# Optimization experiments

Measured on AMD Instinct MI355X. Metric: run time of the kernel, lower is better.

Reference implementation:

```python
import jax, jax.numpy as jnp
import numpy as np

MISSING_VALUE = 128.0
B, T, D, H = 512, 256, 128, 512

def setup_inputs() -> dict:
    key = jax.random.key(0)
    ks = jax.random.split(key, 12)
    x = jax.random.normal(ks[0], (B, T, D), dtype=jnp.float32)
    miss = jax.random.uniform(ks[1], (B, T, D)) < 0.2
    x = jnp.where(miss, jnp.float32(MISSING_VALUE), x)
    tn = lambda k, shp: (jax.random.truncated_normal(k, -2.0, 2.0, shp, jnp.float32) * 0.1)
    # Keras LSTMCell params: kernel [in, 4H], recurrent_kernel [H, 4H], bias [4H] (gate order i,f,c,o)
    k0 = tn(ks[2], (D, 4 * H)); r0 = tn(ks[3], (H, 4 * H)); b0 = jnp.zeros((4 * H,), jnp.float32)
    k1 = tn(ks[4], (H, 4 * H)); r1 = tn(ks[5], (H, 4 * H)); b1 = jnp.zeros((4 * H,), jnp.float32)
    W = tn(ks[6], (H, D))
    b_out = jnp.full((D,), 0.1, jnp.float32)
    return {"x": x, "k0": k0, "r0": r0, "b0": b0, "k1": k1, "r1": r1, "b1": b1, "W": W, "b_out": b_out}

def _lstm_cell(kern, rec, bias, x_in, h, c):
    z = x_in @ kern + h @ rec + bias  # [B, 4H]
    i, f, g, o = jnp.split(z, 4, axis=-1)
    i = jax.nn.sigmoid(i); f = jax.nn.sigmoid(f); g = jnp.tanh(g); o = jax.nn.sigmoid(o)
    c = f * c + i * g
    h = o * jnp.tanh(c)
    return h, c

def reference(x, k0, r0, b0, k1, r1, b1, W, b_out):
    Bx, Tx, Dx = x.shape
    Hx = r0.shape[0]
    zeros = jnp.zeros((Bx, Hx), x.dtype)
    def step(carry, inp):
        t, x_t = inp
        h0, c0, h1, c1, prev_top = carry
        pred = prev_top @ W + b_out                      # imputation from previous top-layer output
        mask = (x_t == MISSING_VALUE) & (t > 0)          # no imputation at t == 0
        cur = jnp.where(mask, pred, x_t)
        h0, c0 = _lstm_cell(k0, r0, b0, cur, h0, c0)
        h1, c1 = _lstm_cell(k1, r1, b1, h0, h1, c1)
        return (h0, c0, h1, c1, h1), h1
    init = (zeros, zeros, zeros, zeros, zeros)
    _, outs = jax.lax.scan(step, init, (jnp.arange(Tx), jnp.transpose(x, (1, 0, 2))))  # outs: [T, B, H]
    last_cell = outs[-1]
    # tf.concat(outputs[:-1], axis=1) -> [B, (T-1)*H]; reshape -> [B*(T-1), H]
    hid = jnp.transpose(outs[:-1], (1, 0, 2)).reshape(-1, Hx)
    prediction = hid @ W + b_out
    return prediction, last_cell
```

## Files before the change

kernel.cpp:

```cpp
#include <hip/hip_runtime.h>

#define B_ 512
#define T_ 256
#define D_ 128
#define H_ 512

typedef _Float16 f16x8 __attribute__((ext_vector_type(8)));
typedef float f32x4 __attribute__((ext_vector_type(4)));
typedef unsigned long long u64;

__device__ __forceinline__ float sigm(float x) { return 1.f / (1.f + __expf(-x)); }
__device__ __forceinline__ float tanh_(float x) { return 2.f / (1.f + __expf(-2.f * x)) - 1.f; }

__global__ void k_convert(const float* __restrict__ k0, const float* __restrict__ r0,
                          const float* __restrict__ k1, const float* __restrict__ r1,
                          const float* __restrict__ W,
                          _Float16* __restrict__ wB0T,
                          _Float16* __restrict__ wB1T,
                          _Float16* __restrict__ wWT)
{
    int tid = blockIdx.x * blockDim.x + threadIdx.x;
    int nth = gridDim.x * blockDim.x;
    for (int idx = tid; idx < 640 * 2048; idx += nth) {
        int k = idx >> 11, n = idx & 2047;
        float v = (k < 128) ? k0[k * 2048 + n] : r0[(k - 128) * 2048 + n];
        wB0T[n * 640 + k] = (_Float16)v;
    }
    for (int idx = tid; idx < 1024 * 2048; idx += nth) {
        int k = idx >> 11, n = idx & 2047;
        float v = (k < 512) ? k1[k * 2048 + n] : r1[(k - 512) * 2048 + n];
        wB1T[n * 1024 + k] = (_Float16)v;
    }
    for (int idx = tid; idx < 512 * 128; idx += nth) {
        int k = idx >> 7, n = idx & 127;
        wWT[n * 512 + k] = (_Float16)W[k * 128 + n];
    }
}

__global__ void k_init(const float* __restrict__ x, _Float16* __restrict__ cur,
                       _Float16* __restrict__ h0a, _Float16* __restrict__ h0b,
                       _Float16* __restrict__ h1a, _Float16* __restrict__ h1b,
                       float* __restrict__ c0, float* __restrict__ c1)
{
    int tid = blockIdx.x * blockDim.x + threadIdx.x;
    int nth = gridDim.x * blockDim.x;
    for (int idx = tid; idx < B_ * D_; idx += nth) {
        int b = idx >> 7, d = idx & 127;
        cur[idx] = (_Float16)x[b * (T_ * D_) + d];
    }
    for (int idx = tid; idx < B_ * H_; idx += nth) {
        h0a[idx] = (_Float16)0.f; h0b[idx] = (_Float16)0.f;
        h1a[idx] = (_Float16)0.f; h1b[idx] = (_Float16)0.f;
        c0[idx] = 0.f; c1[idx] = 0.f;
    }
}

template <int KTOT, int K1>
__global__ __launch_bounds__(512) void k_layer(
    const _Float16* __restrict__ A1, int lda1,
    const _Float16* __restrict__ A2, int lda2,
    const _Float16* __restrict__ BT,
    const float* __restrict__ bias,
    float* __restrict__ cst,
    _Float16* __restrict__ hout,
    float* __restrict__ hout_f32)
{
    constexpr int LSTR = 144;
    __shared__ __align__(16) char smem[2 * 64 * LSTR * 2];
    _Float16* sA = (_Float16*)smem;
    _Float16* sB = sA + 64 * LSTR;
    float* szred = (float*)smem;

    const int j0 = blockIdx.x * 16;
    const int m0 = blockIdx.y * 64;
    const int tid = threadIdx.x;
    const int lane = tid & 63;
    const int wave = tid >> 6;
    const int wpair = wave >> 1;
    const int ksub = wave & 1;

    const int srow = tid >> 3;
    const int skc = (tid & 7) << 4;
    const int swz = (srow & 7) << 3;
    const int sw1 = srow * LSTR + (skc ^ swz);
    const int sw2 = srow * LSTR + ((skc + 8) ^ swz);
    const int bgrow = (srow >> 4) * 512 + j0 + (srow & 15);

    uint4 rA0, rA1, rB0, rB1;
    auto loadA = [&](int kb) {
        int k = kb + skc;
        const _Float16* a; size_t off;
        if (k < K1) { a = A1; off = (size_t)(m0 + srow) * lda1 + k; }
        else        { a = A2; off = (size_t)(m0 + srow) * lda2 + (k - K1); }
        rA0 = *reinterpret_cast<const uint4*>(a + off);
        rA1 = *reinterpret_cast<const uint4*>(a + off + 8);
    };
    auto loadB = [&](int kb) {
        size_t off = (size_t)bgrow * KTOT + kb + skc;
        rB0 = *reinterpret_cast<const uint4*>(BT + off);
        rB1 = *reinterpret_cast<const uint4*>(BT + off + 8);
    };

    loadA(0); loadB(0);

    f32x4 acc[4] = {};
    const int arow = wpair * 16 + (lane & 15);
    const int abase = arow * LSTR;
    const int aswz = (arow & 7) << 3;
    const int kfrag = ksub * 64 + ((lane >> 4) << 3);

    for (int kb = 0; kb < KTOT; kb += 128) {
        __syncthreads();
        *reinterpret_cast<uint4*>(&sA[sw1]) = rA0;
        *reinterpret_cast<uint4*>(&sA[sw2]) = rA1;
        *reinterpret_cast<uint4*>(&sB[sw1]) = rB0;
        *reinterpret_cast<uint4*>(&sB[sw2]) = rB1;
        if (kb + 128 < KTOT) { loadA(kb + 128); loadB(kb + 128); }
        __syncthreads();
#pragma unroll
        for (int kk = 0; kk < 2; ++kk) {
            int ko = kfrag + kk * 32;
            f16x8 a = *reinterpret_cast<const f16x8*>(&sA[abase + (ko ^ aswz)]);
#pragma unroll
            for (int g = 0; g < 4; ++g) {
                int br = g * 16 + (lane & 15);
                f16x8 b = *reinterpret_cast<const f16x8*>(&sB[br * LSTR + (ko ^ ((br & 7) << 3))]);
                acc[g] = __builtin_amdgcn_mfma_f32_16x16x32_f16(b, a, acc[g], 0, 0, 0);
            }
        }
    }

    __syncthreads();
    if (ksub == 1) {
        float* zr = &szred[(wpair * 64 + lane) * 21];
#pragma unroll
        for (int g = 0; g < 4; ++g)
#pragma unroll
            for (int r = 0; r < 4; ++r)
                zr[g * 4 + r] = acc[g][r];
    }
    __syncthreads();
    if (ksub == 0) {
        const int row  = m0 + wpair * 16 + (lane & 15);
        const int colb = j0 + ((lane >> 4) << 2);
        const float* zr = &szred[(wpair * 64 + lane) * 21];
        f32x4 bi4 = *reinterpret_cast<const f32x4*>(&bias[colb]);
        f32x4 bf4 = *reinterpret_cast<const f32x4*>(&bias[512 + colb]);
        f32x4 bg4 = *reinterpret_cast<const f32x4*>(&bias[1024 + colb]);
        f32x4 bo4 = *reinterpret_cast<const f32x4*>(&bias[1536 + colb]);
        f32x4 c4 = *reinterpret_cast<f32x4*>(&cst[row * H_ + colb]);
        union { _Float16 h[4]; u64 u; } hh;
        f32x4 h4;
#pragma unroll
        for (int r = 0; r < 4; ++r) {
            float zi = acc[0][r] + zr[0 + r] + bi4[r];
            float zf = acc[1][r] + zr[4 + r] + bf4[r];
            float zg = acc[2][r] + zr[8 + r] + bg4[r];
            float zo = acc[3][r] + zr[12 + r] + bo4[r];
            float gi = sigm(zi), gf = sigm(zf), gg = tanh_(zg), go = sigm(zo);
            float c = gf * c4[r] + gi * gg;
            c4[r] = c;
            float h = go * tanh_(c);
            h4[r] = h;
            hh.h[r] = (_Float16)h;
        }
        *reinterpret_cast<f32x4*>(&cst[row * H_ + colb]) = c4;
        *reinterpret_cast<u64*>(&hout[row * H_ + colb]) = hh.u;
        if (hout_f32) *reinterpret_cast<f32x4*>(&hout_f32[row * H_ + colb]) = h4;
    }
}

__global__ __launch_bounds__(512) void k_pred(
    const _Float16* __restrict__ h1prev,
    const _Float16* __restrict__ WT,
    const float* __restrict__ bout,
    const float* __restrict__ x,
    int t,
    _Float16* __restrict__ cur,
    float* __restrict__ outPred)
{
    __shared__ float sred[512 * 5];

    const int tid = threadIdx.x;
    const int wave = tid >> 6, l = tid & 63;
    const int pr = blockIdx.x >> 3;
    const int pc = blockIdx.x & 7;
    const int arow = (pr * 16 + (l & 15)) * 512;
    const int brow = (pc * 16 + (l & 15)) * 512;
    const int kof = (l >> 4) << 3;

    f32x4 acc = {};
#pragma unroll
    for (int kk = 0; kk < 2; ++kk) {
        int k = wave * 64 + kk * 32 + kof;
        f16x8 a = *reinterpret_cast<const f16x8*>(h1prev + arow + k);
        f16x8 b = *reinterpret_cast<const f16x8*>(WT + brow + k);
        acc = __builtin_amdgcn_mfma_f32_16x16x32_f16(b, a, acc, 0, 0, 0);
    }
    {
        float* sr = &sred[(wave * 64 + l) * 5];
#pragma unroll
        for (int r = 0; r < 4; ++r) sr[r] = acc[r];
    }
    __syncthreads();
    if (wave == 0) {
#pragma unroll
        for (int w = 1; w < 8; ++w) {
            const float* sr = &sred[(w * 64 + l) * 5];
#pragma unroll
            for (int r = 0; r < 4; ++r) acc[r] += sr[r];
        }
        const int b = pr * 16 + (l & 15);
        const int colb = pc * 16 + ((l >> 4) << 2);
        f32x4 bo4 = *reinterpret_cast<const f32x4*>(&bout[colb]);
        f32x4 xv4 = *reinterpret_cast<const f32x4*>(&x[((size_t)b * T_ + t) * D_ + colb]);
        f32x4 p4;
        union { _Float16 h[4]; u64 u; } ch;
#pragma unroll
        for (int r = 0; r < 4; ++r) {
            float pred = acc[r] + bo4[r];
            p4[r] = pred;
            float cv = (xv4[r] == 128.0f) ? pred : xv4[r];
            ch.h[r] = (_Float16)cv;
        }
        *reinterpret_cast<f32x4*>(&outPred[((size_t)b * (T_ - 1) + (t - 1)) * D_ + colb]) = p4;
        *reinterpret_cast<u64*>(&cur[b * D_ + colb]) = ch.u;
    }
}

extern "C" void kernel_launch(void* const* d_in, const int* in_sizes, int n_in,
                              void* d_out, int out_size, void* d_ws, size_t ws_size,
                              hipStream_t stream)
{
    const float* x  = (const float*)d_in[0];
    const float* k0 = (const float*)d_in[1];
    const float* r0 = (const float*)d_in[2];
    const float* b0 = (const float*)d_in[3];
    const float* k1 = (const float*)d_in[4];
    const float* r1 = (const float*)d_in[5];
    const float* b1 = (const float*)d_in[6];
    const float* W  = (const float*)d_in[7];
    const float* bo = (const float*)d_in[8];
    float* out = (float*)d_out;

    char* ws = (char*)d_ws;
    size_t off = 0;
    auto alloc = [&](size_t bytes) { void* p = ws + off; off += (bytes + 255) & ~255ull; return p; };
    _Float16* wB0T = (_Float16*)alloc((size_t)2048 * 640 * 2);
    _Float16* wB1T = (_Float16*)alloc((size_t)2048 * 1024 * 2);
    _Float16* wWT  = (_Float16*)alloc((size_t)128 * 512 * 2);
    _Float16* cur  = (_Float16*)alloc((size_t)B_ * D_ * 2);
    _Float16* h0[2] = { (_Float16*)alloc((size_t)B_ * H_ * 2), (_Float16*)alloc((size_t)B_ * H_ * 2) };
    _Float16* h1[2] = { (_Float16*)alloc((size_t)B_ * H_ * 2), (_Float16*)alloc((size_t)B_ * H_ * 2) };
    float* c0 = (float*)alloc((size_t)B_ * H_ * 4);
    float* c1 = (float*)alloc((size_t)B_ * H_ * 4);

    k_convert<<<2048, 256, 0, stream>>>(k0, r0, k1, r1, W, wB0T, wB1T, wWT);
    k_init<<<1024, 256, 0, stream>>>(x, cur, h0[0], h0[1], h1[0], h1[1], c0, c1);

    float* lastcell = out + (size_t)B_ * (T_ - 1) * D_;

    for (int t = 0; t < T_; ++t) {
        int cu = t & 1, pv = cu ^ 1;
        if (t > 0)
            k_pred<<<256, 512, 0, stream>>>(h1[pv], wWT, bo, x, t, cur, out);
        k_layer<640, 128><<<dim3(32, 8), 512, 0, stream>>>(
            cur, D_, h0[pv], H_, wB0T, b0, c0, h0[cu], nullptr);
        k_layer<1024, 512><<<dim3(32, 8), 512, 0, stream>>>(
            h0[cu], H_, h1[pv], H_, wB1T, b1, c1, h1[cu],
            (t == T_ - 1) ? lastcell : nullptr);
    }
}
```

Baseline: 5.134 ms.

## Fuse imputation prediction into layer-0 LSTM kernel with redundant per-block compute

Removes the separate prediction kernel and the global cur buffer. Each layer-0 block recomputes the imputation GEMM for its 64 batch rows and writes the imputed input directly into shared memory, and only column-block 0 writes the prediction output. This drops one kernel launch and a global round trip per timestep. In exchange, the small output GEMM is repeated 32 times across blocks and adds a serial prologue before the main loop.

Result: slower. 8.931 ms (+74.0%).

```diff
diff --git a/kernel.cpp b/kernel.cpp
--- a/kernel.cpp
+++ b/kernel.cpp
@@ -37,21 +37,184 @@
     }
 }
 
-__global__ void k_init(const float* __restrict__ x, _Float16* __restrict__ cur,
-                       _Float16* __restrict__ h0a, _Float16* __restrict__ h0b,
+__global__ void k_init(_Float16* __restrict__ h0a, _Float16* __restrict__ h0b,
                        _Float16* __restrict__ h1a, _Float16* __restrict__ h1b,
                        float* __restrict__ c0, float* __restrict__ c1)
 {
     int tid = blockIdx.x * blockDim.x + threadIdx.x;
     int nth = gridDim.x * blockDim.x;
-    for (int idx = tid; idx < B_ * D_; idx += nth) {
-        int b = idx >> 7, d = idx & 127;
-        cur[idx] = (_Float16)x[b * (T_ * D_) + d];
-    }
     for (int idx = tid; idx < B_ * H_; idx += nth) {
         h0a[idx] = (_Float16)0.f; h0b[idx] = (_Float16)0.f;
         h1a[idx] = (_Float16)0.f; h1b[idx] = (_Float16)0.f;
         c0[idx] = 0.f; c1[idx] = 0.f;
+    }
+}
+
+__global__ __launch_bounds__(512) void k_l0(
+    const _Float16* __restrict__ h1prev,
+    const _Float16* __restrict__ h0prev,
+    const _Float16* __restrict__ WT,
+    const _Float16* __restrict__ B0T,
+    const float* __restrict__ bo,
+    const float* __restrict__ bias,
+    const float* __restrict__ x,
+    int t,
+    float* __restrict__ cst,
+    _Float16* __restrict__ hout,
+    float* __restrict__ outPred)
+{
+    constexpr int LSTR = 144;
+    __shared__ __align__(16) char smem[3 * 64 * LSTR * 2];
+    _Float16* sA = (_Float16*)smem;
+    _Float16* sB = sA + 64 * LSTR;
+    _Float16* cuL = sB + 64 * LSTR;
+    float* szred = (float*)smem;
+
+    const int jx = blockIdx.x;
+    const int j0 = jx * 16;
+    const int m0 = blockIdx.y * 64;
+    const int tid = threadIdx.x;
+    const int lane = tid & 63;
+    const int wave = tid >> 6;
+
+    const int srow = tid >> 3;
+    const int skc = (tid & 7) << 4;
+    const int swz = (srow & 7) << 3;
+    const int sw1 = srow * LSTR + (skc ^ swz);
+    const int sw2 = srow * LSTR + ((skc + 8) ^ swz);
+    const int bgrow = (srow >> 4) * 512 + j0 + (srow & 15);
+
+    uint4 rA0, rA1, rB0, rB1;
+    auto loadB = [&](int kb) {
+        size_t off = (size_t)bgrow * 640 + kb + skc;
+        rB0 = *reinterpret_cast<const uint4*>(B0T + off);
+        rB1 = *reinterpret_cast<const uint4*>(B0T + off + 8);
+    };
+    auto loadA = [&](int kb) {
+        size_t off = (size_t)(m0 + srow) * H_ + (kb - 128) + skc;
+        rA0 = *reinterpret_cast<const uint4*>(h0prev + off);
+        rA1 = *reinterpret_cast<const uint4*>(h0prev + off + 8);
+    };
+    loadB(0);
+
+    if (t == 0) {
+        const int rW = tid >> 3;
+        const int kc0 = (tid & 7) * 16;
+        const int cswz = (rW & 7) << 3;
+#pragma unroll
+        for (int h = 0; h < 2; ++h) {
+            int kc = kc0 + h * 8;
+            union { _Float16 f[8]; uint4 q; } v;
+#pragma unroll
+            for (int e = 0; e < 8; ++e)
+                v.f[e] = (_Float16)x[(size_t)(m0 + rW) * T_ * D_ + kc + e];
+            *reinterpret_cast<uint4*>(&cuL[rW * LSTR + (kc ^ cswz)]) = v.q;
+        }
+    } else {
+        const int msub = wave >> 1;
+        const int cbase = (wave & 1) * 4;
+        const int rW = msub * 16 + (lane & 15);
+        const int gb = m0 + rW;
+        const int kof = (lane >> 4) << 3;
+        f32x4 pacc[4] = {};
+        for (int kb = 0; kb < 512; kb += 32) {
+            int k = kb + kof;
+            f16x8 a = *reinterpret_cast<const f16x8*>(h1prev + (size_t)gb * H_ + k);
+#pragma unroll
+            for (int i = 0; i < 4; ++i) {
+                f16x8 b = *reinterpret_cast<const f16x8*>(
+                    WT + (size_t)((cbase + i) * 16 + (lane & 15)) * 512 + k);
+                pacc[i] = __builtin_amdgcn_mfma_f32_16x16x32_f16(b, a, pacc[i], 0, 0, 0);
+            }
+        }
+        const int cswz = (rW & 7) << 3;
+#pragma unroll
+        for (int i = 0; i < 4; ++i) {
+            int colb = (cbase + i) * 16 + ((lane >> 4) << 2);
+            f32x4 bo4 = *reinterpret_cast<const f32x4*>(&bo[colb]);
+            f32x4 xv4 = *reinterpret_cast<const f32x4*>(&x[((size_t)gb * T_ + t) * D_ + colb]);
+            f32x4 p4;
+            union { _Float16 f[4]; u64 u; } cv;
+#pragma unroll
+            for (int r = 0; r < 4; ++r) {
+                float pred = pacc[i][r] + bo4[r];
+                p4[r] = pred;
+                float c = (xv4[r] == 128.0f) ? pred : xv4[r];
+                cv.f[r] = (_Float16)c;
+            }
+            if (jx == 0)
+                *reinterpret_cast<f32x4*>(
+                    &outPred[((size_t)gb * (T_ - 1) + (t - 1)) * D_ + colb]) = p4;
+            *reinterpret_cast<u64*>(
+                &cuL[rW * LSTR + (((colb & ~7) ^ cswz) | (colb & 7))]) = cv.u;
+        }
+    }
+
+    f32x4 acc[4] = {};
+    const int wpair = wave >> 1;
+    const int ksub = wave & 1;
+    const int arow = wpair * 16 + (lane & 15);
+    const int abase = arow * LSTR;
+    const int aswz = (arow & 7) << 3;
+    const int kfrag = ksub * 64 + ((lane >> 4) << 3);
+
+    for (int kb = 0; kb < 640; kb += 128) {
+        __syncthreads();
+        if (kb > 0) {
+            *reinterpret_cast<uint4*>(&sA[sw1]) = rA0;
+            *reinterpret_cast<uint4*>(&sA[sw2]) = rA1;
+        }
+        *reinterpret_cast<uint4*>(&sB[sw1]) = rB0;
+        *reinterpret_cast<uint4*>(&sB[sw2]) = rB1;
+        if (kb + 128 < 640) { loadA(kb + 128); loadB(kb + 128); }
+        __syncthreads();
+        const _Float16* aSrc = (kb == 0) ? cuL : sA;
+#pragma unroll
+        for (int kk = 0; kk < 2; ++kk) {
+            int ko = kfrag + kk * 32;
+            f16x8 a = *reinterpret_cast<const f16x8*>(&aSrc[abase + (ko ^ aswz)]);
+#pragma unroll
+            for (int g = 0; g < 4; ++g) {
+                int br = g * 16 + (lane & 15);
+                f16x8 b = *reinterpret_cast<const f16x8*>(&sB[br * LSTR + (ko ^ ((br & 7) << 3))]);
+                acc[g] = __builtin_amdgcn_mfma_f32_16x16x32_f16(b, a, acc[g], 0, 0, 0);
+            }
+        }
+    }
+
+    __syncthreads();
+    if (ksub == 1) {
+        float* zr = &szred[(wpair * 64 + lane) * 21];
+#pragma unroll
+        for (int g = 0; g < 4; ++g)
+#pragma unroll
+            for (int r = 0; r < 4; ++r)
+                zr[g * 4 + r] = acc[g][r];
+    }
+    __syncthreads();
+    if (ksub == 0) {
+        const int row  = m0 + wpair * 16 + (lane & 15);
+        const int colb = j0 + ((lane >> 4) << 2);
+        const float* zr = &szred[(wpair * 64 + lane) * 21];
+        f32x4 bi4 = *reinterpret_cast<const f32x4*>(&bias[colb]);
+        f32x4 bf4 = *reinterpret_cast<const f32x4*>(&bias[512 + colb]);
+        f32x4 bg4 = *reinterpret_cast<const f32x4*>(&bias[1024 + colb]);
+        f32x4 bo4 = *reinterpret_cast<const f32x4*>(&bias[1536 + colb]);
+        f32x4 c4 = *reinterpret_cast<f32x4*>(&cst[row * H_ + colb]);
+        union { _Float16 h[4]; u64 u; } hh;
+#pragma unroll
+        for (int r = 0; r < 4; ++r) {
+            float zi = acc[0][r] + zr[0 + r] + bi4[r];
+            float zf = acc[1][r] + zr[4 + r] + bf4[r];
+            float zg = acc[2][r] + zr[8 + r] + bg4[r];
+            float zo = acc[3][r] + zr[12 + r] + bo4[r];
+            float gi = sigm(zi), gf = sigm(zf), gg = tanh_(zg), go = sigm(zo);
+            float c = gf * c4[r] + gi * gg;
+            c4[r] = c;
+            hh.h[r] = (_Float16)(go * tanh_(c));
+        }
+        *reinterpret_cast<f32x4*>(&cst[row * H_ + colb]) = c4;
+        *reinterpret_cast<u64*>(&hout[row * H_ + colb]) = hh.u;
     }
 }
 
@@ -170,64 +333,6 @@
     }
 }
 
-__global__ __launch_bounds__(512) void k_pred(
-    const _Float16* __restrict__ h1prev,
-    const _Float16* __restrict__ WT,
-    const float* __restrict__ bout,
-    const float* __restrict__ x,
-    int t,
-    _Float16* __restrict__ cur,
-    float* __restrict__ outPred)
-{
-    __shared__ float sred[512 * 5];
-
-    const int tid = threadIdx.x;
-    const int wave = tid >> 6, l = tid & 63;
-    const int pr = blockIdx.x >> 3;
-    const int pc = blockIdx.x & 7;
-    const int arow = (pr * 16 + (l & 15)) * 512;
-    const int brow = (pc * 16 + (l & 15)) * 512;
-    const int kof = (l >> 4) << 3;
-
-    f32x4 acc = {};
-#pragma unroll
-    for (int kk = 0; kk < 2; ++kk) {
-        int k = wave * 64 + kk * 32 + kof;
-        f16x8 a = *reinterpret_cast<const f16x8*>(h1prev + arow + k);
-        f16x8 b = *reinterpret_cast<const f16x8*>(WT + brow + k);
-        acc = __builtin_amdgcn_mfma_f32_16x16x32_f16(b, a, acc, 0, 0, 0);
-    }
-    {
-        float* sr = &sred[(wave * 64 + l) * 5];
-#pragma unroll
-        for (int r = 0; r < 4; ++r) sr[r] = acc[r];
-    }
-    __syncthreads();
-    if (wave == 0) {
-#pragma unroll
-        for (int w = 1; w < 8; ++w) {
-            const float* sr = &sred[(w * 64 + l) * 5];
-#pragma unroll
-            for (int r = 0; r < 4; ++r) acc[r] += sr[r];
-        }
-        const int b = pr * 16 + (l & 15);
-        const int colb = pc * 16 + ((l >> 4) << 2);
-        f32x4 bo4 = *reinterpret_cast<const f32x4*>(&bout[colb]);
-        f32x4 xv4 = *reinterpret_cast<const f32x4*>(&x[((size_t)b * T_ + t) * D_ + colb]);
-        f32x4 p4;
-        union { _Float16 h[4]; u64 u; } ch;
-#pragma unroll
-        for (int r = 0; r < 4; ++r) {
-            float pred = acc[r] + bo4[r];
-            p4[r] = pred;
-            float cv = (xv4[r] == 128.0f) ? pred : xv4[r];
-            ch.h[r] = (_Float16)cv;
-        }
-        *reinterpret_cast<f32x4*>(&outPred[((size_t)b * (T_ - 1) + (t - 1)) * D_ + colb]) = p4;
-        *reinterpret_cast<u64*>(&cur[b * D_ + colb]) = ch.u;
-    }
-}
-
 extern "C" void kernel_launch(void* const* d_in, const int* in_sizes, int n_in,
                               void* d_out, int out_size, void* d_ws, size_t ws_size,
                               hipStream_t stream)
@@ -249,23 +354,20 @@
     _Float16* wB0T = (_Float16*)alloc((size_t)2048 * 640 * 2);
     _Float16* wB1T = (_Float16*)alloc((size_t)2048 * 1024 * 2);
     _Float16* wWT  = (_Float16*)alloc((size_t)128 * 512 * 2);
-    _Float16* cur  = (_Float16*)alloc((size_t)B_ * D_ * 2);
     _Float16* h0[2] = { (_Float16*)alloc((size_t)B_ * H_ * 2), (_Float16*)alloc((size_t)B_ * H_ * 2) };
     _Float16* h1[2] = { (_Float16*)alloc((size_t)B_ * H_ * 2), (_Float16*)alloc((size_t)B_ * H_ * 2) };
     float* c0 = (float*)alloc((size_t)B_ * H_ * 4);
     float* c1 = (float*)alloc((size_t)B_ * H_ * 4);
 
     k_convert<<<2048, 256, 0, stream>>>(k0, r0, k1, r1, W, wB0T, wB1T, wWT);
-    k_init<<<1024, 256, 0, stream>>>(x, cur, h0[0], h0[1], h1[0], h1[1], c0, c1);
+    k_init<<<1024, 256, 0, stream>>>(h0[0], h0[1], h1[0], h1[1], c0, c1);
 
     float* lastcell = out + (size_t)B_ * (T_ - 1) * D_;
 
     for (int t = 0; t < T_; ++t) {
         int cu = t & 1, pv = cu ^ 1;
-        if (t > 0)
-            k_pred<<<256, 512, 0, stream>>>(h1[pv], wWT, bo, x, t, cur, out);
-        k_layer<640, 128><<<dim3(32, 8), 512, 0, stream>>>(
-            cur, D_, h0[pv], H_, wB0T, b0, c0, h0[cu], nullptr);
+        k_l0<<<dim3(32, 8), 512, 0, stream>>>(
+            h1[pv], h0[pv], wWT, wB0T, bo, b0, x, t, c0, h0[cu], out);
         k_layer<1024, 512><<<dim3(32, 8), 512, 0, stream>>>(
             h0[cu], H_, h1[pv], H_, wB1T, b1, c1, h1[cu],
             (t == T_ - 1) ? lastcell : nullptr);
```
